# Optimization experiments

Measured on AMD Instinct MI355X. Metric: run time of the kernel, lower is better.

## Reference

```python
import jax, jax.numpy as jnp
import numpy as np


def conv2d(x, w, b, pad):
    out = jax.lax.conv_general_dilated(x, w, (1, 1), [(pad, pad), (pad, pad)],
                                       dimension_numbers=('NCHW', 'OIHW', 'NCHW'))
    if b is not None:
        out = out + b[None, :, None, None]
    return out


def propagate(x, conv1_w, conv1_b, res_ws, conv2_w, conv2_b):
    # conv_1 (k3,p1) -> ResidualStack -> relu -> conv_2 (k1)
    y = conv2d(x, conv1_w, conv1_b, 1)
    for w1, w2 in res_ws:
        h = conv2d(jax.nn.relu(y), w1, None, 1)   # 3x3, no bias
        h = conv2d(jax.nn.relu(h), w2, None, 0)   # 1x1, no bias
        y = y + h
    y = jax.nn.relu(y)
    return conv2d(y, conv2_w, conv2_b, 0)


def hopfield_q(y, patterns):
    # HopfieldLayer with static stored/state patterns: attention over learned pattern bank
    B, C, H, W = y.shape
    t = y.transpose(0, 2, 3, 1).reshape(B, H * W, C)                 # tokens [B,HW,C]
    logits = t @ patterns.T / jnp.sqrt(jnp.asarray(C, t.dtype))      # [B,HW,E]
    q = jax.nn.softmax(logits, axis=-1) @ patterns                   # [B,HW,C]
    return q.reshape(B, H, W, C).transpose(0, 3, 1, 2)


def setup_inputs() -> dict:
    key = jax.random.key(0)
    ks = jax.random.split(key, 10)
    B, Cin, Cout, H, RH, E = 8, 64, 32, 8, 32, 512
    s = 0.1  # keep the relu/conv stack numerically tame
    return {
        'x':        jax.random.normal(ks[0], (B, Cin, H, H), jnp.float32),
        'conv1_w':  s * jax.random.normal(ks[1], (Cin, Cin, 3, 3), jnp.float32),
        'conv1_b':  s * jax.random.normal(ks[2], (Cin,), jnp.float32),
        'res0_w1':  s * jax.random.normal(ks[3], (RH, Cin, 3, 3), jnp.float32),
        'res0_w2':  s * jax.random.normal(ks[4], (Cin, RH, 1, 1), jnp.float32),
        'res1_w1':  s * jax.random.normal(ks[5], (RH, Cin, 3, 3), jnp.float32),
        'res1_w2':  s * jax.random.normal(ks[6], (Cin, RH, 1, 1), jnp.float32),
        'conv2_w':  s * jax.random.normal(ks[7], (Cout, Cin, 1, 1), jnp.float32),
        'conv2_b':  s * jax.random.normal(ks[8], (Cout,), jnp.float32),
        'patterns': jax.random.normal(ks[9], (E, Cout), jnp.float32),
    }


def reference(x, conv1_w, conv1_b, res0_w1, res0_w2, res1_w1, res1_w2, conv2_w, conv2_b, patterns):
    res_ws = ((res0_w1, res0_w2), (res1_w1, res1_w2))
    B, Cin, H, W = x.shape
    Cout = conv2_w.shape[0]
    P = H * W  # square images: out_repres_dim == in_repres_dim == H

    def prop1(x1):  # per-sample propagate: [Cin,H,W] -> [Cout,H,W]
        return propagate(x1[None], conv1_w, conv1_b, res_ws, conv2_w, conv2_b)[0]

    def qerr1(x1):  # per-sample quantization error: [Cin,H,W] -> [H,W]
        y = prop1(x1)
        yq = jax.lax.stop_gradient(hopfield_q(y[None], patterns)[0])  # y_quant.detach()
        return ((y - yq) ** 2).sum(axis=0)

    # batch samples are independent, so per-sample jacobians == diagonal blocks used by torch
    e_jac = jax.vmap(jax.jacrev(qerr1))(x)    # [B,H,W,Cin,H,W]
    xy_jac = jax.vmap(jax.jacrev(prop1))(x)   # [B,Cout,H,W,Cin,H,W]

    e_total = e_jac.sum(axis=3).reshape(B, P, P)   # sum over Cin -> [B, out2, in2]
    idx = jnp.argmin(e_total, axis=1)              # [B, in2] routed output pixel per input pixel

    J = xy_jac.reshape(B, Cout, P, Cin, P)         # [B, Cout, out2, Cin, in2]
    x_flat = x.reshape(B, Cin, P)
    onehot = jax.nn.one_hot(idx, P, dtype=x.dtype)  # [B, in2, out2]
    # gather J at routed pixel m, contract x over Cin, scatter-add into m:
    # y_masked[b,o,m] = sum_i onehot[b,i,m] * sum_c x[b,c,i] * J[b,o,m,c,i]
    y_masked = jnp.einsum('bomci,bci,bim->bom', J, x_flat, onehot)

    return hopfield_q(y_masked.reshape(B, Cout, H, W), patterns)
```

## Files before the change

kernel.cpp:

```cpp
#include <hip/hip_runtime.h>
#include <math.h>


constexpr int OFF_MBIT = 0;
constexpr int OFF_N    = 3072;
constexpr int OFF_G    = OFF_N    + 32768;
constexpr int OFF_Y    = OFF_G    + 16384;
constexpr int OFF_X1W  = OFF_Y    + 16384;
constexpr int OFF_WSUM = OFF_X1W  + 294912;
constexpr int OFF_W1RT = OFF_WSUM + 640;
constexpr int OFF_W2RT = OFF_W1RT + 36864;
constexpr int OFF_WC2T = OFF_W2RT + 4096;
constexpr int OFF_W1T  = OFF_WC2T + 2048;
constexpr int OFF_T    = OFF_W1T  + 36864;
constexpr int OFF_IDX  = OFF_T    + 1048576;

__device__ __forceinline__ void conv3x3_tile(
    const float* __restrict__ Wg, const int COdim, const int co0,
    const float* __restrict__ Bp, const int ciBase, const int ciN,
    const int lr, const int lc, float acc[4][8])
{
#pragma unroll
  for (int k = 0; k < 9; k++) {
    const int dy = k / 3 - 1, dx = k % 3 - 1;
// ... 43 lines not shown
    const float* __restrict__ Wg, const int COdim, const int co0,
    const float* __restrict__ Bf, const int ciBase, const int ciN,
    const int lr, const int lc, float acc[4][8])
{
  const float* wbase = Wg + ciBase * COdim + co0 + lc * 4;
  const float* bbase = Bf + ciBase * 64 + lr * 8;
#pragma unroll 4
  for (int ci = 0; ci < ciN; ci++) {
    float4 wv = *(const float4*)(wbase + ci * COdim);
    float4 b0 = *(const float4*)(bbase + ci * 64);
    float4 b1 = *(const float4*)(bbase + ci * 64 + 4);
    float bb[8] = {b0.x, b0.y, b0.z, b0.w, b1.x, b1.y, b1.z, b1.w};
    float wj[4] = {wv.x, wv.y, wv.z, wv.w};
#pragma unroll
    for (int j = 0; j < 4; j++)
#pragma unroll
      for (int px = 0; px < 8; px++)
        acc[j][px] = fmaf(wj[j], bb[px], acc[j][px]);
  }
}

__device__ __forceinline__ void store_tile(float* dst, int lr, int lc,
                                           const float acc[4][8])
{
#pragma unroll
  for (int j = 0; j < 4; j++) {
    *(float4*)(dst + (lc * 4 + j) * 64 + lr * 8) =
        make_float4(acc[j][0], acc[j][1], acc[j][2], acc[j][3]);
    *(float4*)(dst + (lc * 4 + j) * 64 + lr * 8 + 4) =
        make_float4(acc[j][4], acc[j][5], acc[j][6], acc[j][7]);
  }
}

__global__ __launch_bounds__(1024) void kW(
    const float* __restrict__ w1, const float* __restrict__ r0w1,
    const float* __restrict__ r0w2, const float* __restrict__ r1w1,
    const float* __restrict__ r1w2, const float* __restrict__ w2, float* ws)
{
  const int t0 = blockIdx.x * 1024 + threadIdx.x;
  const int stride = gridDim.x * 1024;
  for (int e = t0; e < 36864; e += stride) {
    int co = e & 63, ci = (e >> 6) & 63, k = e >> 12;
    ws[OFF_W1T + e] = w1[(co * 64 + ci) * 9 + k];
  }
  for (int e = t0; e < 18432; e += stride) {
    int co = e & 31, ci = (e >> 5) & 63, k = e >> 11;
    ws[OFF_W1RT + e]         = r0w1[(co * 64 + ci) * 9 + k];
    ws[OFF_W1RT + 18432 + e] = r1w1[(co * 64 + ci) * 9 + k];
  }
  for (int e = t0; e < 2048; e += stride) {
    int co = e & 63, ci = e >> 6;
    ws[OFF_W2RT + e]        = r0w2[co * 32 + ci];
    ws[OFF_W2RT + 2048 + e] = r1w2[co * 32 + ci];
    int o = e & 31, c2 = e >> 5;
    ws[OFF_WC2T + e] = w2[o * 64 + c2];
  }
  for (int e = t0; e < 576; e += stride) {
    int k = e >> 6, co = e & 63;
    float a = 0.f;
    for (int ci = 0; ci < 64; ci++) a += w1[(co * 64 + ci) * 9 + k];
    ws[OFF_WSUM + e] = a;
  }
}

__global__ __launch_bounds__(256) void kX(const float* __restrict__ x,
                                          const float* __restrict__ wsc,
                                          float* ws)
{
  const int bk = blockIdx.x, b = bk / 9, k = bk % 9;
  const int t = threadIdx.x, w = t >> 6, lane = t & 63;
  const int lr = lane >> 3, lc = lane & 7;
  __shared__ __align__(16) float Xp[5120];
  __shared__ __align__(16) float Pq[8192];
  for (int e = t; e < 4096; e += 256) {
    int ci = e >> 6, p = e & 63;
    Xp[ci * 80 + 8 + p] = x[b * 4096 + e];
  }
  __syncthreads();
  float acc[4][8];
#pragma unroll
  for (int j = 0; j < 4; j++)
#pragma unroll
    for (int px = 0; px < 8; px++) acc[j][px] = 0.f;
  const int cohalf = w & 1, ks = w >> 1;
  conv1x1_tile(wsc + OFF_W1T + k * 4096, 64, cohalf * 32, Xp, ks * 32, 32, lr, lc, acc);
  store_tile(Pq + ks * 4096 + cohalf * 2048, lr, lc, acc);
  __syncthreads();
  for (int e = t; e < 4096; e += 256) {
    int co = e & 63, i = e >> 6;
    int pin = (co >> 5) * 2048 + (co & 31) * 64 + i;
    ws[OFF_X1W + ((b * 64 + i) * 9 + k) * 64 + co] = Pq[pin] + Pq[4096 + pin];
  }
}

__global__ __launch_bounds__(1024) void kF(
    const float* __restrict__ b1, const float* __restrict__ b2,
    const float* __restrict__ wsc, float* ws)
{
  const int b = blockIdx.x, t = threadIdx.x;
  const int w = t >> 6, lane = t & 63, lr = lane >> 3, lc = lane & 7;
  __shared__ __align__(16) float Apad[5120];
  __shared__ __align__(16) float Yl[4096];
  __shared__ __align__(16) float Pq[16384];
  __shared__ __align__(16) float Hpad[2560];
  unsigned int* wsi = (unsigned int*)ws;

  if (t < 1024) {
    int ci = t >> 4, r9 = (t >> 3) & 1, c = t & 7;
    Apad[ci * 80 + r9 * 72 + c] = 0.f;
  }
  if (t < 512) {
    int ci = t >> 4, r9 = (t >> 3) & 1, c = t & 7;
    Hpad[ci * 80 + r9 * 72 + c] = 0.f;
  }

  {
    const int co4 = t & 15, p = t >> 4;
    const int py = p >> 3, px = p & 7;
    float4 a = ((const float4*)b1)[co4];
#pragma unroll
    for (int k = 0; k < 9; k++) {
      int dy = k / 3 - 1, dx = k % 3 - 1;
      int qy = py + dy, qx = px + dx;
      if ((unsigned)qy < 8u && (unsigned)qx < 8u) {
        int ik = qy * 8 + qx;
        float4 v = *(const float4*)(wsc + OFF_X1W + ((b * 64 + ik) * 9 + k) * 64 + co4 * 4);
        a.x += v.x; a.y += v.y; a.z += v.z; a.w += v.w;
      }
    }
    float av[4] = {a.x, a.y, a.z, a.w};
#pragma unroll
    for (int j = 0; j < 4; j++) {
      int co = co4 * 4 + j;
      Yl[co * 64 + p] = av[j];
      Apad[co * 80 + 8 + p] = fmaxf(av[j], 0.f);
    }
  }
  __syncthreads();
  if (t < 64) {
    unsigned int lo = 0, hi = 0;
#pragma unroll
    for (int ci = 0; ci < 32; ci++) lo |= (Yl[ci * 64 + t] > 0.f ? 1u : 0u) << ci;
#pragma unroll
    for (int ci = 0; ci < 32; ci++) hi |= (Yl[(32 + ci) * 64 + t] > 0.f ? 1u : 0u) << ci;
    wsi[OFF_MBIT + ((b * 3 + 0) * 64 + t) * 2]     = lo;
    wsi[OFF_MBIT + ((b * 3 + 0) * 64 + t) * 2 + 1] = hi;
  }

  float acc[4][8];
  for (int s = 0; s < 2; s++) {
    if (w < 8) {
#pragma unroll
      for (int j = 0; j < 4; j++)
#pragma unroll
        for (int px = 0; px < 8; px++) acc[j][px] = 0.f;
      conv3x3_tile(wsc + OFF_W1RT + s * 18432, 32, 0, Apad, w * 8, 8, lr, lc, acc);
      store_tile(Pq + w * 2048, lr, lc, acc);
    }
    __syncthreads();
    for (int e = t; e < 2048; e += 1024) {
      int rh = e >> 6, p = e & 63;
      float hv = 0.f;
#pragma unroll
      for (int ks = 0; ks < 8; ks++) hv += Pq[ks * 2048 + e];
      ws[OFF_N + (b * 2 + s) * 2048 + e] = hv > 0.f ? 1.f : 0.f;
      Hpad[rh * 80 + 8 + p] = fmaxf(hv, 0.f);
    }
    __syncthreads();
    if (w < 8) {
#pragma unroll
      for (int j = 0; j < 4; j++)
#pragma unroll
        for (int px = 0; px < 8; px++) acc[j][px] = 0.f;
      const int cohalf = w & 1, ks = w >> 1;
      conv1x1_tile(wsc + OFF_W2RT + s * 2048, 64, cohalf * 32, Hpad, ks * 8, 8, lr, lc, acc);
      store_tile(Pq + ks * 4096 + cohalf * 2048, lr, lc, acc);
    }
    __syncthreads();
    for (int e = t; e < 4096; e += 1024) {
      int co = e >> 6, p = e & 63;
      int pin = (co >> 5) * 2048 + (co & 31) * 64 + p;
      float d = 0.f;
#pragma unroll
      for (int ks = 0; ks < 4; ks++) d += Pq[ks * 4096 + pin];
      float ny = Yl[e] + d;
      Yl[e] = ny;
      Apad[co * 80 + 8 + p] = fmaxf(ny, 0.f);
    }
    __syncthreads();
    if (t < 64) {
      unsigned int lo = 0, hi = 0;
#pragma unroll
      for (int ci = 0; ci < 32; ci++) lo |= (Yl[ci * 64 + t] > 0.f ? 1u : 0u) << ci;
#pragma unroll
      for (int ci = 0; ci < 32; ci++) hi |= (Yl[(32 + ci) * 64 + t] > 0.f ? 1u : 0u) << ci;
      wsi[OFF_MBIT + ((b * 3 + 1 + s) * 64 + t) * 2]     = lo;
      wsi[OFF_MBIT + ((b * 3 + 1 + s) * 64 + t) * 2 + 1] = hi;
    }
  }

  if (w < 8) {
#pragma unroll
    for (int j = 0; j < 4; j++)
#pragma unroll
      for (int px = 0; px < 8; px++) acc[j][px] = 0.f;
    conv1x1_tile(wsc + OFF_WC2T, 32, 0, Apad, w * 8, 8, lr, lc, acc);
    store_tile(Pq + w * 2048, lr, lc, acc);
  }
  __syncthreads();
  for (int e = t; e < 2048; e += 1024) {
    int o = e >> 6, p = e & 63;
    float yv = b2[o];
#pragma unroll
    for (int ks = 0; ks < 8; ks++) yv += Pq[ks * 2048 + e];
    ws[OFF_Y + b * 2048 + p * 32 + o] = yv;
  }
}

__global__ __launch_bounds__(64) void kHopG(const float* __restrict__ wsc,
                                            const float* __restrict__ pat,
                                            float* __restrict__ ws)
{
  const int b = blockIdx.x >> 6, tok = blockIdx.x & 63;
  const int lane = threadIdx.x;
  const float* yp = wsc + OFF_Y + b * 2048 + tok * 32;
  float4 ya[8];
#pragma unroll
  for (int r = 0; r < 8; r++) ya[r] = ((const float4*)yp)[r];

  float l[8];
#pragma unroll
  for (int j = 0; j < 8; j++) {
    const float4* pp = (const float4*)(pat + (j * 64 + lane) * 32);
    float lj = 0.f;
#pragma unroll
    for (int c4 = 0; c4 < 8; c4++) {
      float4 pv = pp[c4];
      lj = fmaf(ya[c4].x, pv.x, lj);
      lj = fmaf(ya[c4].y, pv.y, lj);
// ... 23 lines not shown
#pragma unroll
    for (int c4 = 0; c4 < 8; c4++) {
      float4 pv = pp[c4];
      q[c4 * 4 + 0] = fmaf(nj, pv.x, q[c4 * 4 + 0]);
      q[c4 * 4 + 1] = fmaf(nj, pv.y, q[c4 * 4 + 1]);
      q[c4 * 4 + 2] = fmaf(nj, pv.z, q[c4 * 4 + 2]);
      q[c4 * 4 + 3] = fmaf(nj, pv.w, q[c4 * 4 + 3]);
    }
  }
#pragma unroll
  for (int off = 32; off > 0; off >>= 1) {
#pragma unroll
    for (int c = 0; c < 32; c++) q[c] += __shfl_xor(q[c], off, 64);
  }
  if (lane == 0) {
    float invd = 1.f / dsum;
    float yy[32];
#pragma unroll
    for (int c4 = 0; c4 < 8; c4++) {
      yy[c4 * 4 + 0] = ya[c4].x; yy[c4 * 4 + 1] = ya[c4].y;
      yy[c4 * 4 + 2] = ya[c4].z; yy[c4 * 4 + 3] = ya[c4].w;
    }
    float* gp = ws + OFF_G + b * 2048 + tok * 32;
#pragma unroll
    for (int c4 = 0; c4 < 8; c4++)
      *(float4*)(gp + c4 * 4) = make_float4(
          2.f * (yy[c4 * 4 + 0] - q[c4 * 4 + 0] * invd),
          2.f * (yy[c4 * 4 + 1] - q[c4 * 4 + 1] * invd),
          2.f * (yy[c4 * 4 + 2] - q[c4 * 4 + 2] * invd),
          2.f * (yy[c4 * 4 + 3] - q[c4 * 4 + 3] * invd));
  }
}

__global__ __launch_bounds__(128) void kJ(const float* __restrict__ wsc, float* ws)
{
  const int bid = blockIdx.x;
  const int type = bid & 1, i = (bid >> 1) & 63, b = bid >> 7;
  const int t = threadIdx.x;
  const int w = t >> 6, p = t & 63;
  const int lr = p >> 3, lc = p & 7;
  const int py = p >> 3, px = p & 7, iy = i >> 3, ix = i & 7;
  __shared__ __align__(16) float Up[5120];
  __shared__ __align__(16) float Pp[4096];
  const unsigned int* wsi = (const unsigned int*)wsc;

  float Tch[32];
  {
    int kh = iy - py + 1, kw = ix - px + 1;
    bool v0 = (unsigned)kh < 3u && (unsigned)kw < 3u;
    int kidx = v0 ? kh * 3 + kw : 0;
    const float4* s4 = (const float4*)(type
        ? (wsc + OFF_X1W + ((b * 64 + i) * 9 + kidx) * 64)
        : (wsc + OFF_WSUM + kidx * 64)) + w * 8;
#pragma unroll
    for (int c4 = 0; c4 < 8; c4++) {
      float4 tv = s4[c4];
      Tch[c4 * 4 + 0] = v0 ? tv.x : 0.f;
      Tch[c4 * 4 + 1] = v0 ? tv.y : 0.f;
      Tch[c4 * 4 + 2] = v0 ? tv.z : 0.f;
      Tch[c4 * 4 + 3] = v0 ? tv.w : 0.f;
    }
  }

  float accA[4][8];
  for (int s = 0; s < 2; s++) {
    if (s) __syncthreads();
    unsigned int mw = wsi[OFF_MBIT + ((b * 3 + s) * 64 + p) * 2 + w];
#pragma unroll
    for (int c = 0; c < 32; c++)
      Up[(w * 32 + c) * 80 + 8 + p] = ((mw >> c) & 1u) ? Tch[c] : 0.f;
#pragma unroll
    for (int z = 0; z < 8; z++) {
      int e = z * 64 + p;
      int ci = w * 32 + (e >> 4);
      Up[ci * 80 + ((e >> 3) & 1) * 72 + (e & 7)] = 0.f;
    }
#pragma unroll
    for (int j = 0; j < 4; j++)
#pragma unroll
      for (int pq = 0; pq < 8; pq++) accA[j][pq] = 0.f;
    conv3x3_tile(wsc + OFF_W1RT + s * 18432, 32, 0, Up, w * 32, 32, lr, lc, accA);
    store_tile(Pp + w * 2048, lr, lc, accA);
    __syncthreads();
    {
      float4* Pp4 = (float4*)Pp;
      const float4* Np4 = (const float4*)(wsc + OFF_N + (b * 2 + s) * 2048);
#pragma unroll
      for (int z = 0; z < 4; z++) {
        int e4 = z * 128 + t;
        float4 a = Pp4[e4], bq = Pp4[512 + e4], nv = Np4[e4];
        Pp4[e4] = make_float4((a.x + bq.x) * nv.x, (a.y + bq.y) * nv.y,
                              (a.z + bq.z) * nv.z, (a.w + bq.w) * nv.w);
      }
    }
    __syncthreads();
#pragma unroll
    for (int j = 0; j < 4; j++)
#pragma unroll
      for (int pq = 0; pq < 8; pq++) accA[j][pq] = 0.f;
    conv1x1_flat(wsc + OFF_W2RT + s * 2048, 64, w * 32, Pp, 0, 32, lr, lc, accA);
    store_tile(Up + w * 2048, lr, lc, accA);
#pragma unroll
    for (int c = 0; c < 32; c++) Tch[c] += Up[w * 2048 + c * 64 + p];
  }
  __syncthreads();
  {
    unsigned int mw = wsi[OFF_MBIT + ((b * 3 + 2) * 64 + p) * 2 + w];
#pragma unroll
    for (int c = 0; c < 32; c++)
      Up[(w * 32 + c) * 64 + p] = ((mw >> c) & 1u) ? Tch[c] : 0.f;
#pragma unroll
    for (int j = 0; j < 4; j++)
#pragma unroll
      for (int pq = 0; pq < 8; pq++) accA[j][pq] = 0.f;
    conv1x1_flat(wsc + OFF_WC2T, 32, 0, Up, w * 32, 32, lr, lc, accA);
    store_tile(Pp + w * 2048, lr, lc, accA);
  }
  __syncthreads();

  if (type == 0) {
    if (w == 0) {
      const float* gp = wsc + OFF_G + b * 2048 + p * 32;
      float e = 0.f;
#pragma unroll
      for (int o4 = 0; o4 < 8; o4++) {
        float4 gv = *(const float4*)(gp + o4 * 4);
        int o = o4 * 4;
        e = fmaf(gv.x, Pp[(o + 0) * 64 + p] + Pp[2048 + (o + 0) * 64 + p], e);
        e = fmaf(gv.y, Pp[(o + 1) * 64 + p] + Pp[2048 + (o + 1) * 64 + p], e);
        e = fmaf(gv.z, Pp[(o + 2) * 64 + p] + Pp[2048 + (o + 2) * 64 + p], e);
        e = fmaf(gv.w, Pp[(o + 3) * 64 + p] + Pp[2048 + (o + 3) * 64 + p], e);
      }
      float bv = e; int bi = p;
#pragma unroll
      for (int off = 1; off < 64; off <<= 1) {
        float ov = __shfl_xor(bv, off, 64);
        int oi = __shfl_xor(bi, off, 64);
        if (ov < bv || (ov == bv && oi < bi)) { bv = ov; bi = oi; }
      }
      if (p == 0) ((int*)(ws + OFF_IDX))[b * 64 + i] = bi;
    }
  } else {
    float* Tp = ws + OFF_T + (b * 64 + i) * 2048;
#pragma unroll
    for (int z = 0; z < 4; z++) {
      int e4 = z * 128 + t;
      int m = e4 >> 3, o0 = (e4 & 7) * 4;
      *(float4*)(Tp + e4 * 4) = make_float4(
          Pp[(o0 + 0) * 64 + m] + Pp[2048 + (o0 + 0) * 64 + m],
          Pp[(o0 + 1) * 64 + m] + Pp[2048 + (o0 + 1) * 64 + m],
          Pp[(o0 + 2) * 64 + m] + Pp[2048 + (o0 + 2) * 64 + m],
          Pp[(o0 + 3) * 64 + m] + Pp[2048 + (o0 + 3) * 64 + m]);
    }
  }
}

__global__ __launch_bounds__(64) void kQ(const float* __restrict__ wsc,
                                         const float* __restrict__ pat,
                                         float* __restrict__ outp)
{
  const int b = blockIdx.x >> 6, tok = blockIdx.x & 63;
  const int lane = threadIdx.x;
  const int sidx = ((const int*)(wsc + OFF_IDX))[b * 64 + lane];
  const bool sel = (sidx == tok);
  float ym[32];
  const float4* Tp = (const float4*)(wsc + OFF_T + ((b * 64 + lane) * 64 + tok) * 32);
#pragma unroll
  for (int c4 = 0; c4 < 8; c4++) {
    float4 tv = Tp[c4];
    ym[c4 * 4 + 0] = sel ? tv.x : 0.f;
    ym[c4 * 4 + 1] = sel ? tv.y : 0.f;
    ym[c4 * 4 + 2] = sel ? tv.z : 0.f;
    ym[c4 * 4 + 3] = sel ? tv.w : 0.f;
  }
#pragma unroll
  for (int off = 1; off < 64; off <<= 1) {
#pragma unroll
    for (int c = 0; c < 32; c++) ym[c] += __shfl_xor(ym[c], off, 64);
  }
  float l[8];
#pragma unroll
  for (int j = 0; j < 8; j++) {
    const float4* pp = (const float4*)(pat + (j * 64 + lane) * 32);
    float lj = 0.f;
#pragma unroll
// ... 32 lines not shown
      q[c4 * 4 + 3] = fmaf(nj, pv.w, q[c4 * 4 + 3]);
    }
  }
#pragma unroll
  for (int off = 32; off > 0; off >>= 1) {
#pragma unroll
    for (int c = 0; c < 32; c++) q[c] += __shfl_xor(q[c], off, 64);
  }
  if (lane == 0) {
    float invd = 1.f / dsum;
#pragma unroll
    for (int c = 0; c < 32; c++)
      outp[b * 2048 + c * 64 + tok] = q[c] * invd;
  }
}

extern "C" void kernel_launch(void* const* d_in, const int* in_sizes, int n_in,
                              void* d_out, int out_size, void* d_ws, size_t ws_size,
                              hipStream_t stream) {
  (void)in_sizes; (void)n_in; (void)out_size; (void)ws_size;
  const float* x    = (const float*)d_in[0];
  const float* w1   = (const float*)d_in[1];
  const float* b1   = (const float*)d_in[2];
  const float* r0w1 = (const float*)d_in[3];
  const float* r0w2 = (const float*)d_in[4];
  const float* r1w1 = (const float*)d_in[5];
  const float* r1w2 = (const float*)d_in[6];
  const float* w2   = (const float*)d_in[7];
  const float* b2   = (const float*)d_in[8];
  const float* pat  = (const float*)d_in[9];
  float* ws  = (float*)d_ws;
  float* out = (float*)d_out;

  kW<<<32, 1024, 0, stream>>>(w1, r0w1, r0w2, r1w1, r1w2, w2, ws);
  kX<<<72, 256, 0, stream>>>(x, ws, ws);
  kF<<<8, 1024, 0, stream>>>(b1, b2, ws, ws);
  kHopG<<<512, 64, 0, stream>>>(ws, pat, ws);
  kJ<<<1024, 128, 0, stream>>>(ws, ws);
  kQ<<<512, 64, 0, stream>>>(ws, pat, out);
}
```

Baseline: 279.1 us.

## Double kJ block threads with split-K reduction and stage kF weights in LDS

kJ now runs 256 threads per block. Each wave handles 16 input channels instead of 32, and the partial sums are reduced through a larger LDS buffer, which halves per-thread serial work and register use and adds more waves for latency hiding. kF copies the 3x3 residual weights into shared memory before the conv, and its idle waves prefetch the 1x1 weights into LDS in parallel. The cost is extra barriers and extra LDS traffic for the partial-sum reductions.

```diff
diff --git a/kernel.cpp b/kernel.cpp
--- a/kernel.cpp
+++ b/kernel.cpp
@@ -168,8 +168,10 @@
   const int w = t >> 6, lane = t & 63, lr = lane >> 3, lc = lane & 7;
   __shared__ __align__(16) float Apad[5120];
   __shared__ __align__(16) float Yl[4096];
-  __shared__ __align__(16) float Pq[16384];
+  __shared__ __align__(16) float Pq[18432];
   __shared__ __align__(16) float Hpad[2560];
+  __shared__ __align__(16) float Wsm[2048];
+  __shared__ __align__(16) float Wsm2[2048];
   unsigned int* wsi = (unsigned int*)ws;
 
   if (t < 1024) {
@@ -216,14 +218,30 @@
 
   float acc[4][8];
   for (int s = 0; s < 2; s++) {
+    {
+      const float2* src = (const float2*)(wsc + OFF_W1RT + s * 18432);
+      float2* dst = (float2*)Pq;
+#pragma unroll
+      for (int z = 0; z < 9; z++) dst[z * 1024 + t] = src[z * 1024 + t];
+    }
+    __syncthreads();
     if (w < 8) {
 #pragma unroll
       for (int j = 0; j < 4; j++)
 #pragma unroll
         for (int px = 0; px < 8; px++) acc[j][px] = 0.f;
-      conv3x3_tile(wsc + OFF_W1RT + s * 18432, 32, 0, Apad, w * 8, 8, lr, lc, acc);
-      store_tile(Pq + w * 2048, lr, lc, acc);
-    }
+      conv3x3_tile(Pq, 32, 0, Apad, w * 8, 8, lr, lc, acc);
+    } else {
+      int tt = t - 512;
+#pragma unroll
+      for (int z = 0; z < 4; z++) Wsm[z * 512 + tt] = wsc[OFF_W2RT + s * 2048 + z * 512 + tt];
+      if (s == 1) {
+#pragma unroll
+        for (int z = 0; z < 4; z++) Wsm2[z * 512 + tt] = wsc[OFF_WC2T + z * 512 + tt];
+      }
+    }
+    __syncthreads();
+    if (w < 8) store_tile(Pq + w * 2048, lr, lc, acc);
     __syncthreads();
     for (int e = t; e < 2048; e += 1024) {
       int rh = e >> 6, p = e & 63;
@@ -240,7 +258,7 @@
 #pragma unroll
         for (int px = 0; px < 8; px++) acc[j][px] = 0.f;
       const int cohalf = w & 1, ks = w >> 1;
-      conv1x1_tile(wsc + OFF_W2RT + s * 2048, 64, cohalf * 32, Hpad, ks * 8, 8, lr, lc, acc);
+      conv1x1_tile(Wsm, 64, cohalf * 32, Hpad, ks * 8, 8, lr, lc, acc);
       store_tile(Pq + ks * 4096 + cohalf * 2048, lr, lc, acc);
     }
     __syncthreads();
@@ -271,7 +289,7 @@
     for (int j = 0; j < 4; j++)
 #pragma unroll
       for (int px = 0; px < 8; px++) acc[j][px] = 0.f;
-    conv1x1_tile(wsc + OFF_WC2T, 32, 0, Apad, w * 8, 8, lr, lc, acc);
+    conv1x1_tile(Wsm2, 32, 0, Apad, w * 8, 8, lr, lc, acc);
     store_tile(Pq + w * 2048, lr, lc, acc);
   }
   __syncthreads();
@@ -361,7 +379,7 @@
   }
 }
 
-__global__ __launch_bounds__(128) void kJ(const float* __restrict__ wsc, float* ws)
+__global__ __launch_bounds__(256) void kJ(const float* __restrict__ wsc, float* ws)
 {
   const int bid = blockIdx.x;
   const int type = bid & 1, i = (bid >> 1) & 63, b = bid >> 7;
@@ -370,81 +388,96 @@
   const int lr = p >> 3, lc = p & 7;
   const int py = p >> 3, px = p & 7, iy = i >> 3, ix = i & 7;
   __shared__ __align__(16) float Up[5120];
-  __shared__ __align__(16) float Pp[4096];
+  __shared__ __align__(16) float Pp[8192];
   const unsigned int* wsi = (const unsigned int*)wsc;
 
-  float Tch[32];
+  float Tq[16];
   {
     int kh = iy - py + 1, kw = ix - px + 1;
     bool v0 = (unsigned)kh < 3u && (unsigned)kw < 3u;
     int kidx = v0 ? kh * 3 + kw : 0;
     const float4* s4 = (const float4*)(type
         ? (wsc + OFF_X1W + ((b * 64 + i) * 9 + kidx) * 64)
-        : (wsc + OFF_WSUM + kidx * 64)) + w * 8;
-#pragma unroll
-    for (int c4 = 0; c4 < 8; c4++) {
+        : (wsc + OFF_WSUM + kidx * 64)) + w * 4;
+#pragma unroll
+    for (int c4 = 0; c4 < 4; c4++) {
       float4 tv = s4[c4];
-      Tch[c4 * 4 + 0] = v0 ? tv.x : 0.f;
-      Tch[c4 * 4 + 1] = v0 ? tv.y : 0.f;
-      Tch[c4 * 4 + 2] = v0 ? tv.z : 0.f;
-      Tch[c4 * 4 + 3] = v0 ? tv.w : 0.f;
-    }
-  }
-
-  float accA[4][8];
+      Tq[c4 * 4 + 0] = v0 ? tv.x : 0.f;
+      Tq[c4 * 4 + 1] = v0 ? tv.y : 0.f;
+      Tq[c4 * 4 + 2] = v0 ? tv.z : 0.f;
+      Tq[c4 * 4 + 3] = v0 ? tv.w : 0.f;
+    }
+  }
+
+  float acc[4][8];
   for (int s = 0; s < 2; s++) {
-    if (s) __syncthreads();
-    unsigned int mw = wsi[OFF_MBIT + ((b * 3 + s) * 64 + p) * 2 + w];
-#pragma unroll
-    for (int c = 0; c < 32; c++)
-      Up[(w * 32 + c) * 80 + 8 + p] = ((mw >> c) & 1u) ? Tch[c] : 0.f;
-#pragma unroll
-    for (int z = 0; z < 8; z++) {
-      int e = z * 64 + p;
-      int ci = w * 32 + (e >> 4);
-      Up[ci * 80 + ((e >> 3) & 1) * 72 + (e & 7)] = 0.f;
-    }
+    {
+      unsigned int mword = wsi[OFF_MBIT + ((b * 3 + s) * 64 + p) * 2 + (w >> 1)];
+      unsigned int mq = (mword >> ((w & 1) * 16)) & 0xFFFFu;
+#pragma unroll
+      for (int c = 0; c < 16; c++)
+        Up[(16 * w + c) * 80 + 8 + p] = ((mq >> c) & 1u) ? Tq[c] : 0.f;
+#pragma unroll
+      for (int z = 0; z < 4; z++) {
+        int e = z * 64 + p;
+        int ci = 16 * w + (e >> 4);
+        Up[ci * 80 + ((e >> 3) & 1) * 72 + (e & 7)] = 0.f;
+      }
+    }
+    __syncthreads();
 #pragma unroll
     for (int j = 0; j < 4; j++)
 #pragma unroll
-      for (int pq = 0; pq < 8; pq++) accA[j][pq] = 0.f;
-    conv3x3_tile(wsc + OFF_W1RT + s * 18432, 32, 0, Up, w * 32, 32, lr, lc, accA);
-    store_tile(Pp + w * 2048, lr, lc, accA);
+      for (int pq = 0; pq < 8; pq++) acc[j][pq] = 0.f;
+    conv3x3_tile(wsc + OFF_W1RT + s * 18432, 32, 0, Up, w * 16, 16, lr, lc, acc);
+    store_tile(Pp + w * 2048, lr, lc, acc);
     __syncthreads();
     {
-      float4* Pp4 = (float4*)Pp;
       const float4* Np4 = (const float4*)(wsc + OFF_N + (b * 2 + s) * 2048);
-#pragma unroll
-      for (int z = 0; z < 4; z++) {
-        int e4 = z * 128 + t;
-        float4 a = Pp4[e4], bq = Pp4[512 + e4], nv = Np4[e4];
-        Pp4[e4] = make_float4((a.x + bq.x) * nv.x, (a.y + bq.y) * nv.y,
-                              (a.z + bq.z) * nv.z, (a.w + bq.w) * nv.w);
+      const float4* Pp4 = (const float4*)Pp;
+      float4* V4 = (float4*)Up;
+#pragma unroll
+      for (int z = 0; z < 2; z++) {
+        int e4 = z * 256 + t;
+        float4 a = Pp4[e4], bq = Pp4[512 + e4], c4 = Pp4[1024 + e4], d4 = Pp4[1536 + e4];
+        float4 nv = Np4[e4];
+        V4[e4] = make_float4((a.x + bq.x + c4.x + d4.x) * nv.x,
+                             (a.y + bq.y + c4.y + d4.y) * nv.y,
+                             (a.z + bq.z + c4.z + d4.z) * nv.z,
+                             (a.w + bq.w + c4.w + d4.w) * nv.w);
       }
     }
     __syncthreads();
 #pragma unroll
     for (int j = 0; j < 4; j++)
 #pragma unroll
-      for (int pq = 0; pq < 8; pq++) accA[j][pq] = 0.f;
-    conv1x1_flat(wsc + OFF_W2RT + s * 2048, 64, w * 32, Pp, 0, 32, lr, lc, accA);
-    store_tile(Up + w * 2048, lr, lc, accA);
-#pragma unroll
-    for (int c = 0; c < 32; c++) Tch[c] += Up[w * 2048 + c * 64 + p];
+      for (int pq = 0; pq < 8; pq++) acc[j][pq] = 0.f;
+    conv1x1_flat(wsc + OFF_W2RT + s * 2048, 64, (w >> 1) * 32, Up, (w & 1) * 16, 16, lr, lc, acc);
+    store_tile(Pp + w * 2048, lr, lc, acc);
+    __syncthreads();
+    {
+      const int base0 = (w >> 1) * 2 * 2048, base1 = base0 + 2048;
+      const int coL0 = (w & 1) * 16;
+#pragma unroll
+      for (int c = 0; c < 16; c++)
+        Tq[c] += Pp[base0 + (coL0 + c) * 64 + p] + Pp[base1 + (coL0 + c) * 64 + p];
+    }
+  }
+
+  {
+    unsigned int mword = wsi[OFF_MBIT + ((b * 3 + 2) * 64 + p) * 2 + (w >> 1)];
+    unsigned int mq = (mword >> ((w & 1) * 16)) & 0xFFFFu;
+#pragma unroll
+    for (int c = 0; c < 16; c++)
+      Up[(16 * w + c) * 64 + p] = ((mq >> c) & 1u) ? Tq[c] : 0.f;
   }
   __syncthreads();
-  {
-    unsigned int mw = wsi[OFF_MBIT + ((b * 3 + 2) * 64 + p) * 2 + w];
-#pragma unroll
-    for (int c = 0; c < 32; c++)
-      Up[(w * 32 + c) * 64 + p] = ((mw >> c) & 1u) ? Tch[c] : 0.f;
-#pragma unroll
-    for (int j = 0; j < 4; j++)
-#pragma unroll
-      for (int pq = 0; pq < 8; pq++) accA[j][pq] = 0.f;
-    conv1x1_flat(wsc + OFF_WC2T, 32, 0, Up, w * 32, 32, lr, lc, accA);
-    store_tile(Pp + w * 2048, lr, lc, accA);
-  }
+#pragma unroll
+  for (int j = 0; j < 4; j++)
+#pragma unroll
+    for (int pq = 0; pq < 8; pq++) acc[j][pq] = 0.f;
+  conv1x1_flat(wsc + OFF_WC2T, 32, 0, Up, w * 16, 16, lr, lc, acc);
+  store_tile(Pp + w * 2048, lr, lc, acc);
   __syncthreads();
 
   if (type == 0) {
@@ -455,10 +488,14 @@
       for (int o4 = 0; o4 < 8; o4++) {
         float4 gv = *(const float4*)(gp + o4 * 4);
         int o = o4 * 4;
-        e = fmaf(gv.x, Pp[(o + 0) * 64 + p] + Pp[2048 + (o + 0) * 64 + p], e);
-        e = fmaf(gv.y, Pp[(o + 1) * 64 + p] + Pp[2048 + (o + 1) * 64 + p], e);
-        e = fmaf(gv.z, Pp[(o + 2) * 64 + p] + Pp[2048 + (o + 2) * 64 + p], e);
-        e = fmaf(gv.w, Pp[(o + 3) * 64 + p] + Pp[2048 + (o + 3) * 64 + p], e);
+        float s0 = Pp[(o+0)*64+p] + Pp[2048+(o+0)*64+p] + Pp[4096+(o+0)*64+p] + Pp[6144+(o+0)*64+p];
+        float s1 = Pp[(o+1)*64+p] + Pp[2048+(o+1)*64+p] + Pp[4096+(o+1)*64+p] + Pp[6144+(o+1)*64+p];
+        float s2 = Pp[(o+2)*64+p] + Pp[2048+(o+2)*64+p] + Pp[4096+(o+2)*64+p] + Pp[6144+(o+2)*64+p];
+        float s3 = Pp[(o+3)*64+p] + Pp[2048+(o+3)*64+p] + Pp[4096+(o+3)*64+p] + Pp[6144+(o+3)*64+p];
+        e = fmaf(gv.x, s0, e);
+        e = fmaf(gv.y, s1, e);
+        e = fmaf(gv.z, s2, e);
+        e = fmaf(gv.w, s3, e);
       }
       float bv = e; int bi = p;
 #pragma unroll
@@ -472,14 +509,14 @@
   } else {
     float* Tp = ws + OFF_T + (b * 64 + i) * 2048;
 #pragma unroll
-    for (int z = 0; z < 4; z++) {
-      int e4 = z * 128 + t;
+    for (int z = 0; z < 2; z++) {
+      int e4 = z * 256 + t;
       int m = e4 >> 3, o0 = (e4 & 7) * 4;
-      *(float4*)(Tp + e4 * 4) = make_float4(
-          Pp[(o0 + 0) * 64 + m] + Pp[2048 + (o0 + 0) * 64 + m],
-          Pp[(o0 + 1) * 64 + m] + Pp[2048 + (o0 + 1) * 64 + m],
-          Pp[(o0 + 2) * 64 + m] + Pp[2048 + (o0 + 2) * 64 + m],
-          Pp[(o0 + 3) * 64 + m] + Pp[2048 + (o0 + 3) * 64 + m]);
+      float v[4];
+#pragma unroll
+      for (int j = 0; j < 4; j++)
+        v[j] = Pp[(o0+j)*64+m] + Pp[2048+(o0+j)*64+m] + Pp[4096+(o0+j)*64+m] + Pp[6144+(o0+j)*64+m];
+      *(float4*)(Tp + e4 * 4) = make_float4(v[0], v[1], v[2], v[3]);
     }
   }
 }
@@ -582,6 +619,6 @@
   kX<<<72, 256, 0, stream>>>(x, ws, ws);
   kF<<<8, 1024, 0, stream>>>(b1, b2, ws, ws);
   kHopG<<<512, 64, 0, stream>>>(ws, pat, ws);
-  kJ<<<1024, 128, 0, stream>>>(ws, ws);
+  kJ<<<1024, 256, 0, stream>>>(ws, ws);
   kQ<<<512, 64, 0, stream>>>(ws, pat, out);
 }
```

Measured after the change: 256.8 us. -8.0%, faster.

## Merge weight-transpose and conv1 kernels, stage weights in LDS, slim kJ reductions

Applied to the files above, without the earlier changes.

The weight-transpose kernel is folded into the conv1 input-projection kernel: extra blocks do the remaining transposes, and the conv1 blocks gather their own weight slice into shared memory, which removes one launch. kF now stages the residual 3x3 and 1x1 weights plus the final 1x1 weights in shared memory instead of reading them from global memory inside the conv loops. kJ shrinks its partial-sum buffer by having one warp store its tile and the other add from registers. The argmin energy reduction is also restructured to use register-resident values and fewer shuffles. The cost is extra barriers, more shared memory in kF, and the conv1 blocks recomputing a strided weight gather.

```diff
diff --git a/kernel.cpp b/kernel.cpp
--- a/kernel.cpp
+++ b/kernel.cpp
@@ -99,50 +99,53 @@
   }
 }
 
-__global__ __launch_bounds__(1024) void kW(
-    const float* __restrict__ w1, const float* __restrict__ r0w1,
-    const float* __restrict__ r0w2, const float* __restrict__ r1w1,
-    const float* __restrict__ r1w2, const float* __restrict__ w2, float* ws)
-{
-  const int t0 = blockIdx.x * 1024 + threadIdx.x;
-  const int stride = gridDim.x * 1024;
-  for (int e = t0; e < 36864; e += stride) {
-    int co = e & 63, ci = (e >> 6) & 63, k = e >> 12;
-    ws[OFF_W1T + e] = w1[(co * 64 + ci) * 9 + k];
-  }
-  for (int e = t0; e < 18432; e += stride) {
-    int co = e & 31, ci = (e >> 5) & 63, k = e >> 11;
-    ws[OFF_W1RT + e]         = r0w1[(co * 64 + ci) * 9 + k];
-    ws[OFF_W1RT + 18432 + e] = r1w1[(co * 64 + ci) * 9 + k];
-  }
-  for (int e = t0; e < 2048; e += stride) {
-    int co = e & 63, ci = e >> 6;
-    ws[OFF_W2RT + e]        = r0w2[co * 32 + ci];
-    ws[OFF_W2RT + 2048 + e] = r1w2[co * 32 + ci];
-    int o = e & 31, c2 = e >> 5;
-    ws[OFF_WC2T + e] = w2[o * 64 + c2];
-  }
-  for (int e = t0; e < 576; e += stride) {
-    int k = e >> 6, co = e & 63;
-    float a = 0.f;
-    for (int ci = 0; ci < 64; ci++) a += w1[(co * 64 + ci) * 9 + k];
-    ws[OFF_WSUM + e] = a;
-  }
-}
-
-__global__ __launch_bounds__(256) void kX(const float* __restrict__ x,
-                                          const float* __restrict__ wsc,
-                                          float* ws)
-{
-  const int bk = blockIdx.x, b = bk / 9, k = bk % 9;
-  const int t = threadIdx.x, w = t >> 6, lane = t & 63;
-  const int lr = lane >> 3, lc = lane & 7;
+__global__ __launch_bounds__(256) void kP(
+    const float* __restrict__ x, const float* __restrict__ w1,
+    const float* __restrict__ r0w1, const float* __restrict__ r0w2,
+    const float* __restrict__ r1w1, const float* __restrict__ r1w2,
+    const float* __restrict__ w2, float* ws)
+{
+  const int bk = blockIdx.x;
+  const int t = threadIdx.x;
   __shared__ __align__(16) float Xp[5120];
   __shared__ __align__(16) float Pq[8192];
+  __shared__ __align__(16) float Wk[4096];
+
+  if (bk >= 72) {
+    const int t0 = (bk - 72) * 256 + t;
+    const int stride = 8 * 256;
+    for (int e = t0; e < 18432; e += stride) {
+      int co = e & 31, ci = (e >> 5) & 63, k = e >> 11;
+      ws[OFF_W1RT + e]         = r0w1[(co * 64 + ci) * 9 + k];
+      ws[OFF_W1RT + 18432 + e] = r1w1[(co * 64 + ci) * 9 + k];
+    }
+    for (int e = t0; e < 2048; e += stride) {
+      int co = e & 63, ci = e >> 6;
+      ws[OFF_W2RT + e]        = r0w2[co * 32 + ci];
+      ws[OFF_W2RT + 2048 + e] = r1w2[co * 32 + ci];
+      int o = e & 31, c2 = e >> 5;
+      ws[OFF_WC2T + e] = w2[o * 64 + c2];
+    }
+    for (int e = t0; e < 576; e += stride) {
+      int k = e >> 6, co = e & 63;
+      float a = 0.f;
+      for (int ci = 0; ci < 64; ci++) a += w1[(co * 64 + ci) * 9 + k];
+      ws[OFF_WSUM + e] = a;
+    }
+    return;
+  }
+
+  const int b = bk / 9, k = bk % 9;
+  const int w = t >> 6, lane = t & 63;
+  const int lr = lane >> 3, lc = lane & 7;
   for (int e = t; e < 4096; e += 256) {
     int ci = e >> 6, p = e & 63;
     Xp[ci * 80 + 8 + p] = x[b * 4096 + e];
   }
+  for (int e = t; e < 4096; e += 256) {
+    int ci = e >> 6, co = e & 63;
+    Wk[e] = w1[(co * 64 + ci) * 9 + k];
+  }
   __syncthreads();
   float acc[4][8];
 #pragma unroll
@@ -150,7 +153,7 @@
 #pragma unroll
     for (int px = 0; px < 8; px++) acc[j][px] = 0.f;
   const int cohalf = w & 1, ks = w >> 1;
-  conv1x1_tile(wsc + OFF_W1T + k * 4096, 64, cohalf * 32, Xp, ks * 32, 32, lr, lc, acc);
+  conv1x1_tile(Wk, 64, cohalf * 32, Xp, ks * 32, 32, lr, lc, acc);
   store_tile(Pq + ks * 4096 + cohalf * 2048, lr, lc, acc);
   __syncthreads();
   for (int e = t; e < 4096; e += 256) {
@@ -168,8 +171,10 @@
   const int w = t >> 6, lane = t & 63, lr = lane >> 3, lc = lane & 7;
   __shared__ __align__(16) float Apad[5120];
   __shared__ __align__(16) float Yl[4096];
-  __shared__ __align__(16) float Pq[16384];
+  __shared__ __align__(16) float Pq[18432];
   __shared__ __align__(16) float Hpad[2560];
+  __shared__ __align__(16) float Wsm[2048];
+  __shared__ __align__(16) float Wsm2[2048];
   unsigned int* wsi = (unsigned int*)ws;
 
   if (t < 1024) {
@@ -216,14 +221,30 @@
 
   float acc[4][8];
   for (int s = 0; s < 2; s++) {
+    {
+      const float2* src = (const float2*)(wsc + OFF_W1RT + s * 18432);
+      float2* dst = (float2*)Pq;
+#pragma unroll
+      for (int z = 0; z < 9; z++) dst[z * 1024 + t] = src[z * 1024 + t];
+    }
+    __syncthreads();
     if (w < 8) {
 #pragma unroll
       for (int j = 0; j < 4; j++)
 #pragma unroll
         for (int px = 0; px < 8; px++) acc[j][px] = 0.f;
-      conv3x3_tile(wsc + OFF_W1RT + s * 18432, 32, 0, Apad, w * 8, 8, lr, lc, acc);
-      store_tile(Pq + w * 2048, lr, lc, acc);
-    }
+      conv3x3_tile(Pq, 32, 0, Apad, w * 8, 8, lr, lc, acc);
+    } else {
+      int tt = t - 512;
+#pragma unroll
+      for (int z = 0; z < 4; z++) Wsm[z * 512 + tt] = wsc[OFF_W2RT + s * 2048 + z * 512 + tt];
+      if (s == 1) {
+#pragma unroll
+        for (int z = 0; z < 4; z++) Wsm2[z * 512 + tt] = wsc[OFF_WC2T + z * 512 + tt];
+      }
+    }
+    __syncthreads();
+    if (w < 8) store_tile(Pq + w * 2048, lr, lc, acc);
     __syncthreads();
     for (int e = t; e < 2048; e += 1024) {
       int rh = e >> 6, p = e & 63;
@@ -240,7 +261,7 @@
 #pragma unroll
         for (int px = 0; px < 8; px++) acc[j][px] = 0.f;
       const int cohalf = w & 1, ks = w >> 1;
-      conv1x1_tile(wsc + OFF_W2RT + s * 2048, 64, cohalf * 32, Hpad, ks * 8, 8, lr, lc, acc);
+      conv1x1_tile(Wsm, 64, cohalf * 32, Hpad, ks * 8, 8, lr, lc, acc);
       store_tile(Pq + ks * 4096 + cohalf * 2048, lr, lc, acc);
     }
     __syncthreads();
@@ -271,7 +292,7 @@
     for (int j = 0; j < 4; j++)
 #pragma unroll
       for (int px = 0; px < 8; px++) acc[j][px] = 0.f;
-    conv1x1_tile(wsc + OFF_WC2T, 32, 0, Apad, w * 8, 8, lr, lc, acc);
+    conv1x1_tile(Wsm2, 32, 0, Apad, w * 8, 8, lr, lc, acc);
     store_tile(Pq + w * 2048, lr, lc, acc);
   }
   __syncthreads();
@@ -370,7 +391,7 @@
   const int lr = p >> 3, lc = p & 7;
   const int py = p >> 3, px = p & 7, iy = i >> 3, ix = i & 7;
   __shared__ __align__(16) float Up[5120];
-  __shared__ __align__(16) float Pp[4096];
+  __shared__ __align__(16) float Pv[2048];
   const unsigned int* wsi = (const unsigned int*)wsc;
 
   float Tch[32];
@@ -391,7 +412,7 @@
     }
   }
 
-  float accA[4][8];
+  float acc[4][8];
   for (int s = 0; s < 2; s++) {
     if (s) __syncthreads();
     unsigned int mw = wsi[OFF_MBIT + ((b * 3 + s) * 64 + p) * 2 + w];
@@ -407,62 +428,79 @@
 #pragma unroll
     for (int j = 0; j < 4; j++)
 #pragma unroll
-      for (int pq = 0; pq < 8; pq++) accA[j][pq] = 0.f;
-    conv3x3_tile(wsc + OFF_W1RT + s * 18432, 32, 0, Up, w * 32, 32, lr, lc, accA);
-    store_tile(Pp + w * 2048, lr, lc, accA);
-    __syncthreads();
-    {
-      float4* Pp4 = (float4*)Pp;
-      const float4* Np4 = (const float4*)(wsc + OFF_N + (b * 2 + s) * 2048);
-#pragma unroll
-      for (int z = 0; z < 4; z++) {
-        int e4 = z * 128 + t;
-        float4 a = Pp4[e4], bq = Pp4[512 + e4], nv = Np4[e4];
-        Pp4[e4] = make_float4((a.x + bq.x) * nv.x, (a.y + bq.y) * nv.y,
-                              (a.z + bq.z) * nv.z, (a.w + bq.w) * nv.w);
+      for (int pq = 0; pq < 8; pq++) acc[j][pq] = 0.f;
+    conv3x3_tile(wsc + OFF_W1RT + s * 18432, 32, 0, Up, w * 32, 32, lr, lc, acc);
+    if (w == 1) store_tile(Pv, lr, lc, acc);
+    __syncthreads();
+    if (w == 0) {
+      const float* Np = wsc + OFF_N + (b * 2 + s) * 2048;
+#pragma unroll
+      for (int j = 0; j < 4; j++) {
+        int base = (lc * 4 + j) * 64 + lr * 8;
+#pragma unroll
+        for (int h = 0; h < 2; h++) {
+          float4 pv = *(float4*)(&Pv[base + h * 4]);
+          float4 nv = *(const float4*)(Np + base + h * 4);
+          *(float4*)(&Pv[base + h * 4]) = make_float4(
+              (acc[j][h * 4 + 0] + pv.x) * nv.x,
+              (acc[j][h * 4 + 1] + pv.y) * nv.y,
+              (acc[j][h * 4 + 2] + pv.z) * nv.z,
+              (acc[j][h * 4 + 3] + pv.w) * nv.w);
+        }
       }
     }
     __syncthreads();
 #pragma unroll
     for (int j = 0; j < 4; j++)
 #pragma unroll
-      for (int pq = 0; pq < 8; pq++) accA[j][pq] = 0.f;
-    conv1x1_flat(wsc + OFF_W2RT + s * 2048, 64, w * 32, Pp, 0, 32, lr, lc, accA);
-    store_tile(Up + w * 2048, lr, lc, accA);
+      for (int pq = 0; pq < 8; pq++) acc[j][pq] = 0.f;
+    conv1x1_flat(wsc + OFF_W2RT + s * 2048, 64, w * 32, Pv, 0, 32, lr, lc, acc);
+    store_tile(Up + w * 2048, lr, lc, acc);
 #pragma unroll
     for (int c = 0; c < 32; c++) Tch[c] += Up[w * 2048 + c * 64 + p];
   }
-  __syncthreads();
+
   {
     unsigned int mw = wsi[OFF_MBIT + ((b * 3 + 2) * 64 + p) * 2 + w];
 #pragma unroll
     for (int c = 0; c < 32; c++)
       Up[(w * 32 + c) * 64 + p] = ((mw >> c) & 1u) ? Tch[c] : 0.f;
-#pragma unroll
-    for (int j = 0; j < 4; j++)
-#pragma unroll
-      for (int pq = 0; pq < 8; pq++) accA[j][pq] = 0.f;
-    conv1x1_flat(wsc + OFF_WC2T, 32, 0, Up, w * 32, 32, lr, lc, accA);
-    store_tile(Pp + w * 2048, lr, lc, accA);
-  }
+  }
+  __syncthreads();
+#pragma unroll
+  for (int j = 0; j < 4; j++)
+#pragma unroll
+    for (int pq = 0; pq < 8; pq++) acc[j][pq] = 0.f;
+  conv1x1_flat(wsc + OFF_WC2T, 32, 0, Up, w * 32, 32, lr, lc, acc);
+  if (w == 1) store_tile(Pv, lr, lc, acc);
   __syncthreads();
 
   if (type == 0) {
     if (w == 0) {
-      const float* gp = wsc + OFF_G + b * 2048 + p * 32;
-      float e = 0.f;
-#pragma unroll
-      for (int o4 = 0; o4 < 8; o4++) {
-        float4 gv = *(const float4*)(gp + o4 * 4);
-        int o = o4 * 4;
-        e = fmaf(gv.x, Pp[(o + 0) * 64 + p] + Pp[2048 + (o + 0) * 64 + p], e);
-        e = fmaf(gv.y, Pp[(o + 1) * 64 + p] + Pp[2048 + (o + 1) * 64 + p], e);
-        e = fmaf(gv.z, Pp[(o + 2) * 64 + p] + Pp[2048 + (o + 2) * 64 + p], e);
-        e = fmaf(gv.w, Pp[(o + 3) * 64 + p] + Pp[2048 + (o + 3) * 64 + p], e);
+#pragma unroll
+      for (int j = 0; j < 4; j++) {
+        int base = (lc * 4 + j) * 64 + lr * 8;
+        float4 v0 = *(float4*)(&Pv[base]);
+        float4 v1 = *(float4*)(&Pv[base + 4]);
+        acc[j][0] += v0.x; acc[j][1] += v0.y; acc[j][2] += v0.z; acc[j][3] += v0.w;
+        acc[j][4] += v1.x; acc[j][5] += v1.y; acc[j][6] += v1.z; acc[j][7] += v1.w;
       }
-      float bv = e; int bi = p;
-#pragma unroll
-      for (int off = 1; off < 64; off <<= 1) {
+      float e8[8];
+#pragma unroll
+      for (int pq = 0; pq < 8; pq++) {
+        const float4 gv = *(const float4*)(wsc + OFF_G + b * 2048 + (lr * 8 + pq) * 32 + lc * 4);
+        e8[pq] = gv.x * acc[0][pq] + gv.y * acc[1][pq] + gv.z * acc[2][pq] + gv.w * acc[3][pq];
+      }
+#pragma unroll
+      for (int off = 1; off <= 4; off <<= 1)
+#pragma unroll
+        for (int pq = 0; pq < 8; pq++) e8[pq] += __shfl_xor(e8[pq], off, 64);
+      float bv = e8[0]; int bi = lr * 8;
+#pragma unroll
+      for (int pq = 1; pq < 8; pq++)
+        if (e8[pq] < bv) { bv = e8[pq]; bi = lr * 8 + pq; }
+#pragma unroll
+      for (int off = 8; off <= 32; off <<= 1) {
         float ov = __shfl_xor(bv, off, 64);
         int oi = __shfl_xor(bi, off, 64);
         if (ov < bv || (ov == bv && oi < bi)) { bv = ov; bi = oi; }
@@ -470,16 +508,27 @@
       if (p == 0) ((int*)(ws + OFF_IDX))[b * 64 + i] = bi;
     }
   } else {
+    if (w == 0) {
+#pragma unroll
+      for (int j = 0; j < 4; j++) {
+        int base = (lc * 4 + j) * 64 + lr * 8;
+        float4 v0 = *(float4*)(&Pv[base]);
+        float4 v1 = *(float4*)(&Pv[base + 4]);
+        *(float4*)(&Pv[base]) = make_float4(v0.x + acc[j][0], v0.y + acc[j][1],
+                                            v0.z + acc[j][2], v0.w + acc[j][3]);
+        *(float4*)(&Pv[base + 4]) = make_float4(v1.x + acc[j][4], v1.y + acc[j][5],
+                                                v1.z + acc[j][6], v1.w + acc[j][7]);
+      }
+    }
+    __syncthreads();
     float* Tp = ws + OFF_T + (b * 64 + i) * 2048;
 #pragma unroll
     for (int z = 0; z < 4; z++) {
       int e4 = z * 128 + t;
       int m = e4 >> 3, o0 = (e4 & 7) * 4;
       *(float4*)(Tp + e4 * 4) = make_float4(
-          Pp[(o0 + 0) * 64 + m] + Pp[2048 + (o0 + 0) * 64 + m],
-          Pp[(o0 + 1) * 64 + m] + Pp[2048 + (o0 + 1) * 64 + m],
-          Pp[(o0 + 2) * 64 + m] + Pp[2048 + (o0 + 2) * 64 + m],
-          Pp[(o0 + 3) * 64 + m] + Pp[2048 + (o0 + 3) * 64 + m]);
+          Pv[(o0 + 0) * 64 + m], Pv[(o0 + 1) * 64 + m],
+          Pv[(o0 + 2) * 64 + m], Pv[(o0 + 3) * 64 + m]);
     }
   }
 }
@@ -578,8 +627,7 @@
   float* ws  = (float*)d_ws;
   float* out = (float*)d_out;
 
-  kW<<<32, 1024, 0, stream>>>(w1, r0w1, r0w2, r1w1, r1w2, w2, ws);
-  kX<<<72, 256, 0, stream>>>(x, ws, ws);
+  kP<<<80, 256, 0, stream>>>(x, w1, r0w1, r0w2, r1w1, r1w2, w2, ws);
   kF<<<8, 1024, 0, stream>>>(b1, b2, ws, ws);
   kHopG<<<512, 64, 0, stream>>>(ws, pat, ws);
   kJ<<<1024, 128, 0, stream>>>(ws, ws);
```

Result: faster. 266.3 us (-4.6%).

## Merge weight-transpose kernel into conv prep kernel and stage weights in LDS

Applied to the files above, without the earlier changes.

Removes the separate weight-transposition launch by folding it into the per-(batch,tap) conv kernel: 72 blocks transpose the conv1 weights for their tap directly into shared memory, while 8 extra blocks write the residual and final weights to the workspace. In the fused residual kernel, the 3x3 and 1x1 weights are copied into shared memory before use instead of being read from global memory by every thread, and half the threads prefetch the 1x1 weights while the others compute. This saves one launch and reduces redundant global reads, at the cost of more LDS usage and extra barriers.

```diff
diff --git a/kernel.cpp b/kernel.cpp
--- a/kernel.cpp
+++ b/kernel.cpp
@@ -99,50 +99,53 @@
   }
 }
 
-__global__ __launch_bounds__(1024) void kW(
-    const float* __restrict__ w1, const float* __restrict__ r0w1,
-    const float* __restrict__ r0w2, const float* __restrict__ r1w1,
-    const float* __restrict__ r1w2, const float* __restrict__ w2, float* ws)
-{
-  const int t0 = blockIdx.x * 1024 + threadIdx.x;
-  const int stride = gridDim.x * 1024;
-  for (int e = t0; e < 36864; e += stride) {
-    int co = e & 63, ci = (e >> 6) & 63, k = e >> 12;
-    ws[OFF_W1T + e] = w1[(co * 64 + ci) * 9 + k];
-  }
-  for (int e = t0; e < 18432; e += stride) {
-    int co = e & 31, ci = (e >> 5) & 63, k = e >> 11;
-    ws[OFF_W1RT + e]         = r0w1[(co * 64 + ci) * 9 + k];
-    ws[OFF_W1RT + 18432 + e] = r1w1[(co * 64 + ci) * 9 + k];
-  }
-  for (int e = t0; e < 2048; e += stride) {
-    int co = e & 63, ci = e >> 6;
-    ws[OFF_W2RT + e]        = r0w2[co * 32 + ci];
-    ws[OFF_W2RT + 2048 + e] = r1w2[co * 32 + ci];
-    int o = e & 31, c2 = e >> 5;
-    ws[OFF_WC2T + e] = w2[o * 64 + c2];
-  }
-  for (int e = t0; e < 576; e += stride) {
-    int k = e >> 6, co = e & 63;
-    float a = 0.f;
-    for (int ci = 0; ci < 64; ci++) a += w1[(co * 64 + ci) * 9 + k];
-    ws[OFF_WSUM + e] = a;
-  }
-}
-
-__global__ __launch_bounds__(256) void kX(const float* __restrict__ x,
-                                          const float* __restrict__ wsc,
-                                          float* ws)
-{
-  const int bk = blockIdx.x, b = bk / 9, k = bk % 9;
-  const int t = threadIdx.x, w = t >> 6, lane = t & 63;
-  const int lr = lane >> 3, lc = lane & 7;
+__global__ __launch_bounds__(256) void kP(
+    const float* __restrict__ x, const float* __restrict__ w1,
+    const float* __restrict__ r0w1, const float* __restrict__ r0w2,
+    const float* __restrict__ r1w1, const float* __restrict__ r1w2,
+    const float* __restrict__ w2, float* ws)
+{
+  const int bk = blockIdx.x;
+  const int t = threadIdx.x;
   __shared__ __align__(16) float Xp[5120];
   __shared__ __align__(16) float Pq[8192];
+  __shared__ __align__(16) float Wk[4096];
+
+  if (bk >= 72) {
+    const int t0 = (bk - 72) * 256 + t;
+    const int stride = 8 * 256;
+    for (int e = t0; e < 18432; e += stride) {
+      int co = e & 31, ci = (e >> 5) & 63, k = e >> 11;
+      ws[OFF_W1RT + e]         = r0w1[(co * 64 + ci) * 9 + k];
+      ws[OFF_W1RT + 18432 + e] = r1w1[(co * 64 + ci) * 9 + k];
+    }
+    for (int e = t0; e < 2048; e += stride) {
+      int co = e & 63, ci = e >> 6;
+      ws[OFF_W2RT + e]        = r0w2[co * 32 + ci];
+      ws[OFF_W2RT + 2048 + e] = r1w2[co * 32 + ci];
+      int o = e & 31, c2 = e >> 5;
+      ws[OFF_WC2T + e] = w2[o * 64 + c2];
+    }
+    for (int e = t0; e < 576; e += stride) {
+      int k = e >> 6, co = e & 63;
+      float a = 0.f;
+      for (int ci = 0; ci < 64; ci++) a += w1[(co * 64 + ci) * 9 + k];
+      ws[OFF_WSUM + e] = a;
+    }
+    return;
+  }
+
+  const int b = bk / 9, k = bk % 9;
+  const int w = t >> 6, lane = t & 63;
+  const int lr = lane >> 3, lc = lane & 7;
   for (int e = t; e < 4096; e += 256) {
     int ci = e >> 6, p = e & 63;
     Xp[ci * 80 + 8 + p] = x[b * 4096 + e];
   }
+  for (int e = t; e < 4096; e += 256) {
+    int ci = e >> 6, co = e & 63;
+    Wk[e] = w1[(co * 64 + ci) * 9 + k];
+  }
   __syncthreads();
   float acc[4][8];
 #pragma unroll
@@ -150,7 +153,7 @@
 #pragma unroll
     for (int px = 0; px < 8; px++) acc[j][px] = 0.f;
   const int cohalf = w & 1, ks = w >> 1;
-  conv1x1_tile(wsc + OFF_W1T + k * 4096, 64, cohalf * 32, Xp, ks * 32, 32, lr, lc, acc);
+  conv1x1_tile(Wk, 64, cohalf * 32, Xp, ks * 32, 32, lr, lc, acc);
   store_tile(Pq + ks * 4096 + cohalf * 2048, lr, lc, acc);
   __syncthreads();
   for (int e = t; e < 4096; e += 256) {
@@ -168,8 +171,10 @@
   const int w = t >> 6, lane = t & 63, lr = lane >> 3, lc = lane & 7;
   __shared__ __align__(16) float Apad[5120];
   __shared__ __align__(16) float Yl[4096];
-  __shared__ __align__(16) float Pq[16384];
+  __shared__ __align__(16) float Pq[18432];
   __shared__ __align__(16) float Hpad[2560];
+  __shared__ __align__(16) float Wsm[2048];
+  __shared__ __align__(16) float Wsm2[2048];
   unsigned int* wsi = (unsigned int*)ws;
 
   if (t < 1024) {
@@ -216,14 +221,30 @@
 
   float acc[4][8];
   for (int s = 0; s < 2; s++) {
+    {
+      const float2* src = (const float2*)(wsc + OFF_W1RT + s * 18432);
+      float2* dst = (float2*)Pq;
+#pragma unroll
+      for (int z = 0; z < 9; z++) dst[z * 1024 + t] = src[z * 1024 + t];
+    }
+    __syncthreads();
     if (w < 8) {
 #pragma unroll
       for (int j = 0; j < 4; j++)
 #pragma unroll
         for (int px = 0; px < 8; px++) acc[j][px] = 0.f;
-      conv3x3_tile(wsc + OFF_W1RT + s * 18432, 32, 0, Apad, w * 8, 8, lr, lc, acc);
-      store_tile(Pq + w * 2048, lr, lc, acc);
-    }
+      conv3x3_tile(Pq, 32, 0, Apad, w * 8, 8, lr, lc, acc);
+    } else {
+      int tt = t - 512;
+#pragma unroll
+      for (int z = 0; z < 4; z++) Wsm[z * 512 + tt] = wsc[OFF_W2RT + s * 2048 + z * 512 + tt];
+      if (s == 1) {
+#pragma unroll
+        for (int z = 0; z < 4; z++) Wsm2[z * 512 + tt] = wsc[OFF_WC2T + z * 512 + tt];
+      }
+    }
+    __syncthreads();
+    if (w < 8) store_tile(Pq + w * 2048, lr, lc, acc);
     __syncthreads();
     for (int e = t; e < 2048; e += 1024) {
       int rh = e >> 6, p = e & 63;
@@ -240,7 +261,7 @@
 #pragma unroll
         for (int px = 0; px < 8; px++) acc[j][px] = 0.f;
       const int cohalf = w & 1, ks = w >> 1;
-      conv1x1_tile(wsc + OFF_W2RT + s * 2048, 64, cohalf * 32, Hpad, ks * 8, 8, lr, lc, acc);
+      conv1x1_tile(Wsm, 64, cohalf * 32, Hpad, ks * 8, 8, lr, lc, acc);
       store_tile(Pq + ks * 4096 + cohalf * 2048, lr, lc, acc);
     }
     __syncthreads();
@@ -271,7 +292,7 @@
     for (int j = 0; j < 4; j++)
 #pragma unroll
       for (int px = 0; px < 8; px++) acc[j][px] = 0.f;
-    conv1x1_tile(wsc + OFF_WC2T, 32, 0, Apad, w * 8, 8, lr, lc, acc);
+    conv1x1_tile(Wsm2, 32, 0, Apad, w * 8, 8, lr, lc, acc);
     store_tile(Pq + w * 2048, lr, lc, acc);
   }
   __syncthreads();
@@ -578,8 +599,7 @@
   float* ws  = (float*)d_ws;
   float* out = (float*)d_out;
 
-  kW<<<32, 1024, 0, stream>>>(w1, r0w1, r0w2, r1w1, r1w2, w2, ws);
-  kX<<<72, 256, 0, stream>>>(x, ws, ws);
+  kP<<<80, 256, 0, stream>>>(x, w1, r0w1, r0w2, r1w1, r1w2, w2, ws);
   kF<<<8, 1024, 0, stream>>>(b1, b2, ws, ws);
   kHopG<<<512, 64, 0, stream>>>(ws, pat, ws);
   kJ<<<1024, 128, 0, stream>>>(ws, ws);
```

After: 231.1 us. -17.2%, faster.
